# Performance work log

Hardware: AMD Instinct MI355X
Metric: run time of the kernel (lower is better)

The kernel has to match this reference:

```python
import jax, jax.numpy as jnp
import numpy as np

DIM = 512
NUM_HEADS = 8
HEAD_DIM = DIM // NUM_HEADS
EPS = 1e-12  # F.normalize default eps


def _l2norm(x):
    # F.normalize: x / max(||x||_2, eps) along last dim
    n = jnp.sqrt(jnp.sum(x * x, axis=-1, keepdims=True))
    return x / jnp.maximum(n, EPS)


def setup_inputs() -> dict:
    key = jax.random.key(0)
    ks = jax.random.split(key, 7)
    B, N, K = 8, 4096, 256
    scale = 1.0 / np.sqrt(DIM)
    return {
        "X_flat": jax.random.normal(ks[0], (B, N, DIM), jnp.float32),
        "S_tokens": jax.random.normal(ks[1], (B, K, DIM), jnp.float32),
        "Wq": jax.random.normal(ks[2], (DIM, DIM), jnp.float32) * scale,
        "Wk": jax.random.normal(ks[3], (DIM, DIM), jnp.float32) * scale,
        "Wv": jax.random.normal(ks[4], (DIM, DIM), jnp.float32) * scale,
        "Wo": jax.random.normal(ks[5], (DIM, DIM), jnp.float32) * scale,
        "temperature": jnp.ones((NUM_HEADS, 1, 1), jnp.float32),
    }


def reference(X_flat, S_tokens, Wq, Wk, Wv, Wo, temperature):
    B, N, C = X_flat.shape
    K = S_tokens.shape[1]
    H, D = NUM_HEADS, HEAD_DIM
    # torch Linear: y = x @ W.T
    q = (X_flat @ Wq.T).reshape(B, N, H, D).transpose(0, 2, 1, 3)   # (B,H,N,D)
    k = (S_tokens @ Wk.T).reshape(B, K, H, D).transpose(0, 2, 1, 3)  # (B,H,K,D)
    v = (S_tokens @ Wv.T).reshape(B, K, H, D).transpose(0, 2, 1, 3)  # (B,H,K,D)
    q = _l2norm(q)
    k = _l2norm(k)
    attn = jnp.einsum('bhnd,bhkd->bhnk', q, k) * temperature  # temperature (H,1,1) broadcasts
    attn = jax.nn.softmax(attn, axis=-1)
    out = jnp.einsum('bhnk,bhkd->bhnd', attn, v)
    out = out.transpose(0, 2, 1, 3).reshape(B, N, C)
    out = out @ Wo.T
    return X_flat + out
```

## Files before the change

kernel.cpp:

```cpp
#include <hip/hip_runtime.h>
#include <hip/hip_bf16.h>


typedef __bf16 bf16;
typedef __attribute__((ext_vector_type(8))) __bf16 bf16x8;
typedef __attribute__((ext_vector_type(4))) float f32x4;

__device__ __forceinline__ void gload_lds16(const void* g, void* l) {
  __builtin_amdgcn_global_load_lds(
      (__attribute__((address_space(1))) void*)g,
      (__attribute__((address_space(3))) void*)l, 16, 0, 0);
}

__device__ __forceinline__ unsigned pack2(float a, float b) {
  unsigned short x = __builtin_bit_cast(unsigned short, (bf16)a);
  unsigned short y = __builtin_bit_cast(unsigned short, (bf16)b);
  return (unsigned)x | ((unsigned)y << 16);
}

__global__ __launch_bounds__(256) void cvt_all(
    const float* __restrict__ X, const float* __restrict__ S,
    const float* __restrict__ Wq, const float* __restrict__ Wk,
    const float* __restrict__ Wv, const float* __restrict__ Wo,
    bf16* __restrict__ Xb, bf16* __restrict__ Sb, bf16* __restrict__ Wqb,
    bf16* __restrict__ Wkb, bf16* __restrict__ Wvb, bf16* __restrict__ Wob) {
  int i = blockIdx.x * 256 + threadIdx.x;
  const float* src;
  bf16* dst;
  int r;
  if (i < 2097152) {
    src = X; dst = Xb; r = i;
  } else if (i < 2228224) {
    src = S; dst = Sb; r = i - 2097152;
  } else {
    int j = i - 2228224;
    int w = j >> 15;
    r = j & 32767;
    src = (w == 0) ? Wq : (w == 1) ? Wk : (w == 2) ? Wv : Wo;
    dst = (w == 0) ? Wqb : (w == 1) ? Wkb : (w == 2) ? Wvb : Wob;
  }
  float4 a = *(const float4*)(src + (size_t)r * 8);
  float4 b = *(const float4*)(src + (size_t)r * 8 + 4);
  uint4 v;
  v.x = pack2(a.x, a.y);
  v.y = pack2(a.z, a.w);
  v.z = pack2(b.x, b.y);
  v.w = pack2(b.z, b.w);
  *(uint4*)(dst + (size_t)r * 8) = v;
}

__global__ __launch_bounds__(256) void proj_all(
    const bf16* __restrict__ Xb, const bf16* __restrict__ Sb,
    const bf16* __restrict__ Wqb, const bf16* __restrict__ Wkb,
    const bf16* __restrict__ Wvb, bf16* __restrict__ Q,
    bf16* __restrict__ Kn, bf16* __restrict__ Vt) {
  __shared__ __align__(16) char smem[49152];

  const int lg = (blockIdx.x & 7) * 144 + (blockIdx.x >> 3);

  const bf16* A;
  const bf16* W;
  int m0, kind;
  if (lg < 1024) {
    kind = 0; A = Xb; W = Wqb; m0 = (lg >> 2) * 128;
  } else if (lg < 1088) {
    kind = 1; A = Sb; W = Wkb; m0 = ((lg - 1024) >> 2) * 128;
  } else {
    kind = 2; A = Sb; W = Wvb; m0 = ((lg - 1088) >> 2) * 128;
  }
  const int n0 = (lg & 3) * 128;

  const int tid = threadIdx.x;
  const int wid = tid >> 6, lane = tid & 63;
  const int wr = wid >> 1, wc = wid & 1;
  const int g = lane >> 4, c16 = lane & 15;
  const int r0 = tid >> 2, cc0 = tid & 3;
  const int r1 = (256 + tid) >> 2, cc1 = tid & 3;
  const int dst0 = (tid & ~63) * 16, dst1 = (256 + (tid & ~63)) * 16;

  f32x4 acc[4][4] = {};

#define PSTAGE(kb, buf)                                                     \
  {                                                                         \
    char* as = smem + (buf) * 8192;                                         \
    char* bs = smem + 24576 + (buf) * 8192;                                 \
    gload_lds16(A + (size_t)(m0 + r0) * 512 + (kb) + cc0 * 8, as + dst0);   \
    gload_lds16(A + (size_t)(m0 + r1) * 512 + (kb) + cc1 * 8, as + dst1);   \
    gload_lds16(W + (size_t)(n0 + r0) * 512 + (kb) + cc0 * 8, bs + dst0);   \
    gload_lds16(W + (size_t)(n0 + r1) * 512 + (kb) + cc1 * 8, bs + dst1);   \
  }

#define PCOMPUTE(buf)                                                       \
  {                                                                         \
    const bf16* as = (const bf16*)(smem + (buf) * 8192);                    \
    const bf16* bs = (const bf16*)(smem + 24576 + (buf) * 8192);            \
    bf16x8 af[4], bfr[4];                                                   \
    _Pragma("unroll") for (int mi = 0; mi < 4; ++mi) af[mi] =               \
        *(const bf16x8*)(as + (wr * 64 + mi * 16 + c16) * 32 + g * 8);      \
    _Pragma("unroll") for (int ni = 0; ni < 4; ++ni) bfr[ni] =              \
        *(const bf16x8*)(bs + (wc * 64 + ni * 16 + c16) * 32 + g * 8);      \
    _Pragma("unroll") for (int mi = 0; mi < 4; ++mi)                        \
        _Pragma("unroll") for (int ni = 0; ni < 4; ++ni) acc[mi][ni] =      \
            __builtin_amdgcn_mfma_f32_16x16x32_bf16(af[mi], bfr[ni],        \
                                                    acc[mi][ni], 0, 0, 0);  \
  }

  PSTAGE(0, 0);
  PSTAGE(32, 1);
  int bufc = 0;
  for (int t = 0; t < 14; ++t) {
    int bufn = bufc + 2;
    if (bufn >= 3) bufn -= 3;
    PSTAGE((t + 2) * 32, bufn);
    asm volatile("s_waitcnt vmcnt(8)" ::: "memory");
    __builtin_amdgcn_s_barrier();
    PCOMPUTE(bufc);
    __builtin_amdgcn_s_barrier();
    if (++bufc == 3) bufc = 0;
  }
  asm volatile("s_waitcnt vmcnt(4)" ::: "memory");
  __builtin_amdgcn_s_barrier();
  PCOMPUTE(bufc);
  __builtin_amdgcn_s_barrier();
  if (++bufc == 3) bufc = 0;
  asm volatile("s_waitcnt vmcnt(0)" ::: "memory");
  __builtin_amdgcn_s_barrier();
  PCOMPUTE(bufc);

  __syncthreads();

  if (kind != 2) {
    bf16* C = (kind == 0) ? Q : Kn;
    char* eps = smem + wid * 8192;
#pragma unroll
    for (int mi = 0; mi < 4; ++mi) {
      float ss[4];
#pragma unroll
      for (int j = 0; j < 4; ++j) {
        float s = 0.f;
#pragma unroll
        for (int ni = 0; ni < 4; ++ni) {
          float v = acc[mi][ni][j];
          s += v * v;
        }
        ss[j] = s;
      }
#pragma unroll
      for (int msk = 1; msk < 16; msk <<= 1)
#pragma unroll
        for (int j = 0; j < 4; ++j) ss[j] += __shfl_xor(ss[j], msk, 64);
      float inv[4];
#pragma unroll
      for (int j = 0; j < 4; ++j) inv[j] = rsqrtf(fmaxf(ss[j], 1e-24f));
#pragma unroll
      for (int ni = 0; ni < 4; ++ni)
#pragma unroll
        for (int j = 0; j < 4; ++j) {
          int row = mi * 16 + g * 4 + j, col = ni * 16 + c16;
          int off = (row * 128 + col * 2) ^ ((row & 7) << 4);
          *(bf16*)(eps + off) = (bf16)(acc[mi][ni][j] * inv[j]);
        }
    }
    asm volatile("s_waitcnt lgkmcnt(0)" ::: "memory");
#pragma unroll
    for (int it = 0; it < 8; ++it) {
      int c = it * 64 + lane;
      int row = c >> 3, ch = c & 7;
      int off = (row * 128 + ch * 16) ^ ((row & 7) << 4);
      bf16x8 v = *(const bf16x8*)(eps + off);
      *(bf16x8*)(C + (size_t)(m0 + wr * 64 + row) * 512 + n0 + wc * 64 +
                 ch * 8) = v;
    }
  } else {
#pragma unroll
    for (int mi = 0; mi < 4; ++mi) {
      int m = m0 + wr * 64 + mi * 16 + g * 4;
      int b = m >> 8, tt = m & 255;
#pragma unroll
      for (int ni = 0; ni < 4; ++ni) {
        int col = n0 + wc * 64 + ni * 16 + c16;
        int h = col >> 6, d = col & 63;
        uint2 v;
        v.x = pack2(acc[mi][ni][0], acc[mi][ni][1]);
        v.y = pack2(acc[mi][ni][2], acc[mi][ni][3]);
        *(uint2*)(Vt + ((size_t)((b * 8 + h) * 64 + d) * 256 + tt)) = v;
      }
    }
  }
#undef PSTAGE
#undef PCOMPUTE
}

__global__ __launch_bounds__(256) void out_gemm(
    const bf16* __restrict__ O, const bf16* __restrict__ Wob,
    const float* __restrict__ Xres, float* __restrict__ out) {
  __shared__ __align__(16) char smem[49152];

  const int lg = (blockIdx.x & 7) * 128 + (blockIdx.x >> 3);
  const int m0 = (lg >> 2) * 128, n0 = (lg & 3) * 128;

  const int tid = threadIdx.x;
  const int wid = tid >> 6, lane = tid & 63;
  const int wr = wid >> 1, wc = wid & 1;
  const int g = lane >> 4, c16 = lane & 15;
  const int r0 = tid >> 2, cc0 = tid & 3;
  const int r1 = (256 + tid) >> 2, cc1 = tid & 3;
  const int dst0 = (tid & ~63) * 16, dst1 = (256 + (tid & ~63)) * 16;

  f32x4 acc[4][4] = {};

#define OSTAGE(kb, buf)                                                      \
  {                                                                          \
    char* as = smem + (buf) * 8192;                                          \
    char* bs = smem + 24576 + (buf) * 8192;                                  \
    gload_lds16(O + (size_t)(m0 + r0) * 512 + (kb) + cc0 * 8, as + dst0);    \
    gload_lds16(O + (size_t)(m0 + r1) * 512 + (kb) + cc1 * 8, as + dst1);    \
    gload_lds16(Wob + (size_t)(n0 + r0) * 512 + (kb) + cc0 * 8, bs + dst0);  \
    gload_lds16(Wob + (size_t)(n0 + r1) * 512 + (kb) + cc1 * 8, bs + dst1);  \
  }

#define OCOMPUTE(buf)                                                       \
  {                                                                         \
    const bf16* as = (const bf16*)(smem + (buf) * 8192);                    \
    const bf16* bs = (const bf16*)(smem + 24576 + (buf) * 8192);            \
    bf16x8 af[4], bfr[4];                                                   \
    _Pragma("unroll") for (int mi = 0; mi < 4; ++mi) af[mi] =               \
        *(const bf16x8*)(as + (wr * 64 + mi * 16 + c16) * 32 + g * 8);      \
    _Pragma("unroll") for (int ni = 0; ni < 4; ++ni) bfr[ni] =              \
        *(const bf16x8*)(bs + (wc * 64 + ni * 16 + c16) * 32 + g * 8);      \
    _Pragma("unroll") for (int mi = 0; mi < 4; ++mi)                        \
        _Pragma("unroll") for (int ni = 0; ni < 4; ++ni) acc[mi][ni] =      \
            __builtin_amdgcn_mfma_f32_16x16x32_bf16(af[mi], bfr[ni],        \
                                                    acc[mi][ni], 0, 0, 0);  \
  }

  OSTAGE(0, 0);
  OSTAGE(32, 1);
  int bufc = 0;
  for (int t = 0; t < 14; ++t) {
    int bufn = bufc + 2;
    if (bufn >= 3) bufn -= 3;
    OSTAGE((t + 2) * 32, bufn);
    asm volatile("s_waitcnt vmcnt(8)" ::: "memory");
    __builtin_amdgcn_s_barrier();
    OCOMPUTE(bufc);
    __builtin_amdgcn_s_barrier();
    if (++bufc == 3) bufc = 0;
  }
  asm volatile("s_waitcnt vmcnt(4)" ::: "memory");
  __builtin_amdgcn_s_barrier();
  OCOMPUTE(bufc);
  __builtin_amdgcn_s_barrier();
  if (++bufc == 3) bufc = 0;
  asm volatile("s_waitcnt vmcnt(0)" ::: "memory");
  __builtin_amdgcn_s_barrier();
  OCOMPUTE(bufc);

  __syncthreads();

  char* eps = smem + wid * 8192;
#pragma unroll
  for (int p = 0; p < 2; ++p) {
#pragma unroll
    for (int mm = 0; mm < 2; ++mm)
#pragma unroll
      for (int ni = 0; ni < 4; ++ni)
#pragma unroll
        for (int j = 0; j < 4; ++j) {
          int row = mm * 16 + g * 4 + j, col = ni * 16 + c16;
          int off = (row * 256 + col * 4) ^ ((row & 7) << 4);
          *(float*)(eps + off) = acc[p * 2 + mm][ni][j];
        }
    asm volatile("s_waitcnt lgkmcnt(0)" ::: "memory");
#pragma unroll
    for (int it = 0; it < 8; ++it) {
      int c = it * 64 + lane;
      int row = c >> 4, ch = c & 15;
      int off = (row * 256 + ch * 16) ^ ((row & 7) << 4);
      float4 v = *(const float4*)(eps + off);
      size_t gr = (size_t)(m0 + wr * 64 + p * 32 + row) * 512 + n0 +
                  wc * 64 + ch * 4;
      float4 x = *(const float4*)(Xres + gr);
      v.x += x.x;
      v.y += x.y;
      v.z += x.z;
      v.w += x.w;
      *(float4*)(out + gr) = v;
    }
    asm volatile("s_waitcnt lgkmcnt(0)" ::: "memory");
  }
#undef OSTAGE
#undef OCOMPUTE
}

__global__ __launch_bounds__(256) void attn_fused(
    const bf16* __restrict__ Qn, const bf16* __restrict__ Kn,
    const bf16* __restrict__ Vt, const float* __restrict__ temp,
    bf16* __restrict__ O) {
  __shared__ __align__(16) char smem[73728];

  const int tid = threadIdx.x;
  const int w = tid >> 6, lane = tid & 63;
  const int g = lane >> 4, c16 = lane & 15;
  const int lg = (blockIdx.x & 7) * 512 + (blockIdx.x >> 3);
  const int nt = lg & 63, h = (lg >> 6) & 7, b = lg >> 9;
  const int n0 = nt * 64;

  {
    const bf16* Ksrc = Kn + ((size_t)b * 256) * 512 + h * 64;
#pragma unroll
    for (int it = 0; it < 8; ++it) {
      int c = it * 256 + tid;
      int t = c >> 3, dc = c & 7;
      int4 v = *(const int4*)(Ksrc + (size_t)t * 512 + dc * 8);
      int off = (t * 128 + dc * 16) ^ ((t & 7) << 4);
      *(int4*)(smem + off) = v;
    }
    const bf16* Vsrc = Vt + (size_t)((b * 8 + h) * 64) * 256;
#pragma unroll
    for (int it = 0; it < 8; ++it) {
      int c = it * 256 + tid;
      int d = c >> 5, tc = c & 31;
      int4 v = *(const int4*)(Vsrc + (size_t)d * 256 + tc * 8);
      int off = (d * 512 + tc * 16) ^ ((d & 7) << 4);
      *(int4*)(smem + 32768 + off) = v;
    }
    const bf16* Qsrc = Qn + ((size_t)b * 4096 + n0) * 512 + h * 64;
#pragma unroll
    for (int it = 0; it < 2; ++it) {
      int c = it * 256 + tid;
      int q = c >> 3, dc = c & 7;
      int4 v = *(const int4*)(Qsrc + (size_t)q * 512 + dc * 8);
      int off = 65536 + ((q * 128 + dc * 16) ^ ((q & 7) << 4));
      *(int4*)(smem + off) = v;
    }
  }
  __syncthreads();

  const int q = w * 16 + c16;

  f32x4 sacc[16] = {};
  bf16x8 qf[2];
#pragma unroll
  for (int s = 0; s < 2; ++s) {
    int off = 65536 + ((q * 128 + s * 64 + g * 16) ^ ((q & 7) << 4));
    qf[s] = *(const bf16x8*)(smem + off);
  }
#pragma unroll
  for (int mi = 0; mi < 16; ++mi) {
#pragma unroll
    for (int s = 0; s < 2; ++s) {
      int t = mi * 16 + c16;
      int off = (t * 128 + s * 64 + g * 16) ^ ((t & 7) << 4);
      bf16x8 kf = *(const bf16x8*)(smem + off);
      sacc[mi] = __builtin_amdgcn_mfma_f32_16x16x32_bf16(kf, qf[s], sacc[mi],
                                                         0, 0, 0);
    }
  }

  float tv = temp[h];
  float mx4[4] = {-1e30f, -1e30f, -1e30f, -1e30f};
#pragma unroll
  for (int mi = 0; mi < 16; ++mi)
#pragma unroll
    for (int j = 0; j < 4; ++j) {
      sacc[mi][j] *= tv;
      mx4[j] = fmaxf(mx4[j], sacc[mi][j]);
    }
  float mx = fmaxf(fmaxf(mx4[0], mx4[1]), fmaxf(mx4[2], mx4[3]));
  mx = fmaxf(mx, __shfl_xor(mx, 16, 64));
  mx = fmaxf(mx, __shfl_xor(mx, 32, 64));
  float sm4[4] = {0.f, 0.f, 0.f, 0.f};
#pragma unroll
  for (int mi = 0; mi < 16; ++mi)
#pragma unroll
    for (int j = 0; j < 4; ++j) {
      float p = __expf(sacc[mi][j] - mx);
      sacc[mi][j] = p;
      sm4[j] += p;
    }
  float sum = (sm4[0] + sm4[1]) + (sm4[2] + sm4[3]);
  sum += __shfl_xor(sum, 16, 64);
  sum += __shfl_xor(sum, 32, 64);
  float inv = 1.0f / sum;

  __syncthreads();

#pragma unroll
  for (int mi = 0; mi < 16; ++mi) {
    uint2 v;
    v.x = pack2(sacc[mi][0] * inv, sacc[mi][1] * inv);
    v.y = pack2(sacc[mi][2] * inv, sacc[mi][3] * inv);
    int off = (q * 512 + mi * 32 + g * 8) ^ ((q & 7) << 4);
    *(uint2*)(smem + off) = v;
  }
  __syncthreads();

  f32x4 oacc[4] = {};
#pragma unroll
  for (int ks = 0; ks < 8; ++ks) {
    int offa = (q * 512 + ks * 64 + g * 16) ^ ((q & 7) << 4);
    bf16x8 pa = *(const bf16x8*)(smem + offa);
#pragma unroll
    for (int ni = 0; ni < 4; ++ni) {
      int d = ni * 16 + c16;
      int offb = 32768 + ((d * 512 + ks * 64 + g * 16) ^ ((d & 7) << 4));
      bf16x8 vb = *(const bf16x8*)(smem + offb);
      oacc[ni] = __builtin_amdgcn_mfma_f32_16x16x32_bf16(pa, vb, oacc[ni],
                                                         0, 0, 0);
    }
  }

  {
    char* ox = smem + 65536 + w * 2048;
#pragma unroll
    for (int ni = 0; ni < 4; ++ni)
#pragma unroll
      for (int j = 0; j < 4; ++j) {
        int row = g * 4 + j, col = ni * 16 + c16;
        int off = (row * 128 + col * 2) ^ ((row & 7) << 4);
        *(bf16*)(ox + off) = (bf16)oacc[ni][j];
      }
    asm volatile("s_waitcnt lgkmcnt(0)" ::: "memory");
#pragma unroll
    for (int it = 0; it < 2; ++it) {
      int c = it * 64 + lane;
      int row = c >> 3, ch = c & 7;
      int off = (row * 128 + ch * 16) ^ ((row & 7) << 4);
      bf16x8 v = *(const bf16x8*)(ox + off);
      *(bf16x8*)(O + ((size_t)b * 4096 + n0 + w * 16 + row) * 512 + h * 64 +
                 ch * 8) = v;
    }
  }
}

extern "C" void kernel_launch(void* const* d_in, const int* in_sizes, int n_in,
                              void* d_out, int out_size, void* d_ws,
                              size_t ws_size, hipStream_t stream) {
  const float* X = (const float*)d_in[0];
  const float* S = (const float*)d_in[1];
  const float* Wq = (const float*)d_in[2];
  const float* Wk = (const float*)d_in[3];
  const float* Wv = (const float*)d_in[4];
  const float* Wo = (const float*)d_in[5];
  const float* temp = (const float*)d_in[6];
  float* out = (float*)d_out;

  char* ws = (char*)d_ws;
  bf16* Qws = (bf16*)ws;
  bf16* Kws = (bf16*)(ws + 33554432);
  bf16* Vtws = (bf16*)(ws + 35651584);
  bf16* Wqb = (bf16*)(ws + 37748736);
  bf16* Wkb = (bf16*)(ws + 38273024);
  bf16* Wvb = (bf16*)(ws + 38797312);
  bf16* Wob = (bf16*)(ws + 39321600);

  bf16* Xb = (bf16*)d_out;
  bf16* Sb = (bf16*)((char*)d_out + 33554432);

  cvt_all<<<dim3(9216), dim3(256), 0, stream>>>(X, S, Wq, Wk, Wv, Wo, Xb, Sb,
                                                Wqb, Wkb, Wvb, Wob);
  proj_all<<<dim3(1152), dim3(256), 0, stream>>>(Xb, Sb, Wqb, Wkb, Wvb, Qws,
                                                 Kws, Vtws);
  attn_fused<<<dim3(4096), dim3(256), 0, stream>>>(Qws, Kws, Vtws, temp, Qws);
  out_gemm<<<dim3(1024), dim3(256), 0, stream>>>(Qws, Wob, X, out);
}
```

Baseline: 129.6 us.

## Fold temperature into Q, use exp2, async K/V loads, defer softmax normalization

Scales normalized Q by temperature*log2(e) in the projection epilogue so attention can use exp2 without a per-score multiply. K and V tiles are loaded straight into LDS with global_load_lds and pre-swizzled addresses, and Q fragments are read directly into registers, which cuts LDS from 72KB to 64KB. Softmax normalization is moved to the output, and one barrier is dropped because each wave writes only its own P rows. Storing Q pre-scaled in bf16 and unnormalized P in bf16 changes rounding slightly.

```diff
diff --git a/kernel.cpp b/kernel.cpp
--- a/kernel.cpp
+++ b/kernel.cpp
@@ -5,6 +5,12 @@
 typedef __bf16 bf16;
 typedef __attribute__((ext_vector_type(8))) __bf16 bf16x8;
 typedef __attribute__((ext_vector_type(4))) float f32x4;
+
+#if __has_builtin(__builtin_amdgcn_exp2f)
+#define EXP2(x) __builtin_amdgcn_exp2f(x)
+#else
+#define EXP2(x) exp2f(x)
+#endif
 
 __device__ __forceinline__ void gload_lds16(const void* g, void* l) {
   __builtin_amdgcn_global_load_lds(
@@ -52,8 +58,8 @@
 __global__ __launch_bounds__(256) void proj_all(
     const bf16* __restrict__ Xb, const bf16* __restrict__ Sb,
     const bf16* __restrict__ Wqb, const bf16* __restrict__ Wkb,
-    const bf16* __restrict__ Wvb, bf16* __restrict__ Q,
-    bf16* __restrict__ Kn, bf16* __restrict__ Vt) {
+    const bf16* __restrict__ Wvb, const float* __restrict__ temp,
+    bf16* __restrict__ Q, bf16* __restrict__ Kn, bf16* __restrict__ Vt) {
   __shared__ __align__(16) char smem[49152];
 
   const int lg = (blockIdx.x & 7) * 144 + (blockIdx.x >> 3);
@@ -131,6 +137,8 @@
 
   if (kind != 2) {
     bf16* C = (kind == 0) ? Q : Kn;
+    const float sc =
+        (kind == 0) ? temp[(n0 + wc * 64) >> 6] * 1.44269504088896f : 1.0f;
     char* eps = smem + wid * 8192;
 #pragma unroll
     for (int mi = 0; mi < 4; ++mi) {
@@ -151,7 +159,8 @@
         for (int j = 0; j < 4; ++j) ss[j] += __shfl_xor(ss[j], msk, 64);
       float inv[4];
 #pragma unroll
-      for (int j = 0; j < 4; ++j) inv[j] = rsqrtf(fmaxf(ss[j], 1e-24f));
+      for (int j = 0; j < 4; ++j)
+        inv[j] = rsqrtf(fmaxf(ss[j], 1e-24f)) * sc;
 #pragma unroll
       for (int ni = 0; ni < 4; ++ni)
 #pragma unroll
@@ -295,9 +304,8 @@
 
 __global__ __launch_bounds__(256) void attn_fused(
     const bf16* __restrict__ Qn, const bf16* __restrict__ Kn,
-    const bf16* __restrict__ Vt, const float* __restrict__ temp,
-    bf16* __restrict__ O) {
-  __shared__ __align__(16) char smem[73728];
+    const bf16* __restrict__ Vt, bf16* __restrict__ O) {
+  __shared__ __align__(16) char smem[65536];
 
   const int tid = threadIdx.x;
   const int w = tid >> 6, lane = tid & 63;
@@ -308,44 +316,25 @@
 
   {
     const bf16* Ksrc = Kn + ((size_t)b * 256) * 512 + h * 64;
+    const bf16* Vsrc = Vt + (size_t)((b * 8 + h) * 64) * 256;
 #pragma unroll
     for (int it = 0; it < 8; ++it) {
-      int c = it * 256 + tid;
-      int t = c >> 3, dc = c & 7;
-      int4 v = *(const int4*)(Ksrc + (size_t)t * 512 + dc * 8);
-      int off = (t * 128 + dc * 16) ^ ((t & 7) << 4);
-      *(int4*)(smem + off) = v;
-    }
-    const bf16* Vsrc = Vt + (size_t)((b * 8 + h) * 64) * 256;
-#pragma unroll
-    for (int it = 0; it < 8; ++it) {
-      int c = it * 256 + tid;
-      int d = c >> 5, tc = c & 31;
-      int4 v = *(const int4*)(Vsrc + (size_t)d * 256 + tc * 8);
-      int off = (d * 512 + tc * 16) ^ ((d & 7) << 4);
-      *(int4*)(smem + 32768 + off) = v;
-    }
-    const bf16* Qsrc = Qn + ((size_t)b * 4096 + n0) * 512 + h * 64;
-#pragma unroll
-    for (int it = 0; it < 2; ++it) {
-      int c = it * 256 + tid;
-      int q = c >> 3, dc = c & 7;
-      int4 v = *(const int4*)(Qsrc + (size_t)q * 512 + dc * 8);
-      int off = 65536 + ((q * 128 + dc * 16) ^ ((q & 7) << 4));
-      *(int4*)(smem + off) = v;
-    }
-  }
+      int base = it * 256 + w * 64;
+      int c = base + lane;
+      int t = c >> 3, dk = (c & 7) ^ (t & 7);
+      gload_lds16(Ksrc + (size_t)t * 512 + dk * 8, smem + base * 16);
+      int d = c >> 5, tc = (c & 31) ^ (d & 7);
+      gload_lds16(Vsrc + (size_t)d * 256 + tc * 8, smem + 32768 + base * 16);
+    }
+  }
+  const int q = w * 16 + c16;
+  const bf16* Qsrc = Qn + ((size_t)b * 4096 + n0) * 512 + h * 64;
+  bf16x8 qf[2];
+  qf[0] = *(const bf16x8*)(Qsrc + (size_t)q * 512 + g * 8);
+  qf[1] = *(const bf16x8*)(Qsrc + (size_t)q * 512 + 32 + g * 8);
   __syncthreads();
 
-  const int q = w * 16 + c16;
-
   f32x4 sacc[16] = {};
-  bf16x8 qf[2];
-#pragma unroll
-  for (int s = 0; s < 2; ++s) {
-    int off = 65536 + ((q * 128 + s * 64 + g * 16) ^ ((q & 7) << 4));
-    qf[s] = *(const bf16x8*)(smem + off);
-  }
 #pragma unroll
   for (int mi = 0; mi < 16; ++mi) {
 #pragma unroll
@@ -358,15 +347,11 @@
     }
   }
 
-  float tv = temp[h];
   float mx4[4] = {-1e30f, -1e30f, -1e30f, -1e30f};
 #pragma unroll
   for (int mi = 0; mi < 16; ++mi)
 #pragma unroll
-    for (int j = 0; j < 4; ++j) {
-      sacc[mi][j] *= tv;
-      mx4[j] = fmaxf(mx4[j], sacc[mi][j]);
-    }
+    for (int j = 0; j < 4; ++j) mx4[j] = fmaxf(mx4[j], sacc[mi][j]);
   float mx = fmaxf(fmaxf(mx4[0], mx4[1]), fmaxf(mx4[2], mx4[3]));
   mx = fmaxf(mx, __shfl_xor(mx, 16, 64));
   mx = fmaxf(mx, __shfl_xor(mx, 32, 64));
@@ -375,7 +360,7 @@
   for (int mi = 0; mi < 16; ++mi)
 #pragma unroll
     for (int j = 0; j < 4; ++j) {
-      float p = __expf(sacc[mi][j] - mx);
+      float p = EXP2(sacc[mi][j] - mx);
       sacc[mi][j] = p;
       sm4[j] += p;
     }
@@ -389,12 +374,11 @@
 #pragma unroll
   for (int mi = 0; mi < 16; ++mi) {
     uint2 v;
-    v.x = pack2(sacc[mi][0] * inv, sacc[mi][1] * inv);
-    v.y = pack2(sacc[mi][2] * inv, sacc[mi][3] * inv);
+    v.x = pack2(sacc[mi][0], sacc[mi][1]);
+    v.y = pack2(sacc[mi][2], sacc[mi][3]);
     int off = (q * 512 + mi * 32 + g * 8) ^ ((q & 7) << 4);
     *(uint2*)(smem + off) = v;
   }
-  __syncthreads();
 
   f32x4 oacc[4] = {};
 #pragma unroll
@@ -412,14 +396,14 @@
   }
 
   {
-    char* ox = smem + 65536 + w * 2048;
+    char* ox = smem + w * 8192;
 #pragma unroll
     for (int ni = 0; ni < 4; ++ni)
 #pragma unroll
       for (int j = 0; j < 4; ++j) {
         int row = g * 4 + j, col = ni * 16 + c16;
         int off = (row * 128 + col * 2) ^ ((row & 7) << 4);
-        *(bf16*)(ox + off) = (bf16)oacc[ni][j];
+        *(bf16*)(ox + off) = (bf16)(oacc[ni][j] * inv);
       }
     asm volatile("s_waitcnt lgkmcnt(0)" ::: "memory");
 #pragma unroll
@@ -460,8 +444,8 @@
 
   cvt_all<<<dim3(9216), dim3(256), 0, stream>>>(X, S, Wq, Wk, Wv, Wo, Xb, Sb,
                                                 Wqb, Wkb, Wvb, Wob);
-  proj_all<<<dim3(1152), dim3(256), 0, stream>>>(Xb, Sb, Wqb, Wkb, Wvb, Qws,
-                                                 Kws, Vtws);
-  attn_fused<<<dim3(4096), dim3(256), 0, stream>>>(Qws, Kws, Vtws, temp, Qws);
+  proj_all<<<dim3(1152), dim3(256), 0, stream>>>(Xb, Sb, Wqb, Wkb, Wvb, temp,
+                                                 Qws, Kws, Vtws);
+  attn_fused<<<dim3(4096), dim3(256), 0, stream>>>(Qws, Kws, Vtws, Qws);
   out_gemm<<<dim3(1024), dim3(256), 0, stream>>>(Qws, Wob, X, out);
 }
```

Measured after the change: 127.6 us. Within noise of the previous version (-1.5%).
